# Optimization experiments

Measured on AMD Instinct MI355X. Metric: run time of the kernel, lower is better.

The kernel has to match this reference:

```python
import jax, jax.numpy as jnp
import numpy as np
from jax.ops import segment_sum

EPS = 1e-5
N, E = 100000, 1600000
CIN, H, COUT, ED = 32, 64, 16, 16


def _lin(k, fan_in, fan_out):
    return jax.random.normal(k, (fan_in, fan_out), jnp.float32) / np.sqrt(fan_in)


def setup_inputs() -> dict:
    key = jax.random.key(0)
    ks = jax.random.split(key, 24)
    inp = {
        "x": jax.random.normal(ks[0], (N, CIN), jnp.float32),
        "edge_index": jax.random.randint(ks[1], (2, E), 0, N, jnp.int32),
        "edge_attr": jax.random.normal(ks[2], (E, ED), jnp.float32),
    }
    # layer 1 (SAGEConvWithEdgeAttr: in=CIN -> H)
    inp.update(
        l1_Wl=_lin(ks[3], CIN, H), l1_bl=jnp.zeros((H,), jnp.float32),
        l1_Wr=_lin(ks[4], CIN, H),
        l1_We=_lin(ks[5], ED, H), l1_be=jnp.zeros((H,), jnp.float32),
        l1_Wg=_lin(ks[6], 2 * H, H), l1_bg=jnp.zeros((H,), jnp.float32),
        l1_bng=jnp.ones((H,), jnp.float32), l1_bnb=jnp.zeros((H,), jnp.float32),
    )
    # layer 2 (H -> H)
    inp.update(
        l2_Wl=_lin(ks[7], H, H), l2_bl=jnp.zeros((H,), jnp.float32),
        l2_Wr=_lin(ks[8], H, H),
        l2_We=_lin(ks[9], ED, H), l2_be=jnp.zeros((H,), jnp.float32),
        l2_Wg=_lin(ks[10], 2 * H, H), l2_bg=jnp.zeros((H,), jnp.float32),
        l2_bng=jnp.ones((H,), jnp.float32), l2_bnb=jnp.zeros((H,), jnp.float32),
    )
    # GraphNorms (weight=1, bias=0, mean_scale=1 at init; randomize slightly via ones)
    inp.update(
        gn1_g=jnp.ones((H,), jnp.float32), gn1_b=jnp.zeros((H,), jnp.float32), gn1_a=jnp.ones((H,), jnp.float32),
        gn2_g=jnp.ones((H,), jnp.float32), gn2_b=jnp.zeros((H,), jnp.float32), gn2_a=jnp.ones((H,), jnp.float32),
        lin_W=_lin(ks[11], H, COUT), lin_b=jnp.zeros((COUT,), jnp.float32),
    )
    return inp


def _sage_edge_layer(x, row, col, ea, Wl, bl, Wr, We, be, Wg, bg, bng, bnb):
    n = x.shape[0]
    ea_t = ea @ We + be                                        # [E', H]
    deg = segment_sum(jnp.ones_like(col, dtype=x.dtype), col, num_segments=n)
    agg = segment_sum(x[row], col, num_segments=n) / jnp.maximum(deg, 1.0)[:, None]
    out = agg @ Wl + bl + x @ Wr                               # SAGEConv (mean)
    gate = jax.nn.sigmoid(jnp.concatenate([out[col], ea_t], -1) @ Wg + bg)
    out = out + segment_sum(gate * ea_t, col, num_segments=n)  # edge contributions
    mu = out.mean(0)
    var = ((out - mu) ** 2).mean(0)                            # BatchNorm1d (batch stats)
    out = bng * (out - mu) * jax.lax.rsqrt(var + EPS) + bnb
    return jax.nn.relu(2.0 * out)                              # Identity residual + out, relu


def _graph_norm(x, g, b, a):
    mu = x.mean(0)
    xc = x - a * mu
    var = (xc ** 2).mean(0)
    return g * xc * jax.lax.rsqrt(var + EPS) + b


def reference(x, edge_index, edge_attr,
              l1_Wl, l1_bl, l1_Wr, l1_We, l1_be, l1_Wg, l1_bg, l1_bng, l1_bnb,
              l2_Wl, l2_bl, l2_Wr, l2_We, l2_be, l2_Wg, l2_bg, l2_bng, l2_bnb,
              gn1_g, gn1_b, gn1_a, gn2_g, gn2_b, gn2_a, lin_W, lin_b):
    n = x.shape[0]
    loop = jnp.arange(n, dtype=edge_index.dtype)
    row = jnp.concatenate([edge_index[0], loop])               # add_self_loops
    col = jnp.concatenate([edge_index[1], loop])
    ea = jnp.concatenate([edge_attr, jnp.ones((n, edge_attr.shape[1]), edge_attr.dtype)], 0)
    h = _sage_edge_layer(x, row, col, ea, l1_Wl, l1_bl, l1_Wr, l1_We, l1_be, l1_Wg, l1_bg, l1_bng, l1_bnb)
    h = jax.nn.relu(h)
    h = jax.nn.relu(_graph_norm(h, gn1_g, gn1_b, gn1_a))
    h = _sage_edge_layer(h, row, col, ea, l2_Wl, l2_bl, l2_Wr, l2_We, l2_be, l2_Wg, l2_bg, l2_bng, l2_bnb)
    h = jax.nn.relu(h)
    h = jax.nn.relu(_graph_norm(h, gn2_g, gn2_b, gn2_a))
    return h @ lin_W + lin_b
```

## Files before the change

kernel.cpp:

```cpp
#include <hip/hip_runtime.h>
#include <hip/hip_fp16.h>
#include <math.h>
#include <stdint.h>

#define H 64
#define ED 16
#define CO 16
#define WGRID 2048
#define NWAVES (WGRID * 4)
#define CPART 1024
static constexpr float EPSV = 1e-5f;
static constexpr float LOG2E = 1.44269504f;

typedef _Float16 h2v __attribute__((ext_vector_type(2)));
typedef _Float16 f16x8 __attribute__((ext_vector_type(8)));
typedef float f32x4 __attribute__((ext_vector_type(4)));

__device__ __forceinline__ float sigm2(float z) {
    return __builtin_amdgcn_rcpf(1.0f + __builtin_amdgcn_exp2f(-z));
}

__device__ __forceinline__ f16x8 as_f16x8(int4 v) { union { int4 i; f16x8 h; } u; u.i = v; return u.h; }

__device__ __forceinline__ int pack2(float a, float b) {
    __half2 h = __floats2half2_rn(a, b);
    return *reinterpret_cast<int*>(&h);
}

__global__ void k_prep(const float* __restrict__ We1, const float* __restrict__ be1, const float* __restrict__ Wg1,
                       const float* __restrict__ We2, const float* __restrict__ be2, const float* __restrict__ Wg2,
                       float* __restrict__ ws) {
    int j = threadIdx.x;
    for (int l = 0; l < 2; ++l) {
        const float* We = l ? We2 : We1;
        const float* be = l ? be2 : be1;
        const float* Wg = l ? Wg2 : Wg1;
        int* wth = (int*)(ws + (l ? 1024 : 0));
        int* wgh = (int*)(ws + (l ? 1536 : 512));
        float* ets = ws + 2048 + l * 192;
        float* vs  = ws + 2112 + l * 192;
        float* dv  = ws + 2176 + l * 192;
        float wt[ED], wg[ED];
        float et = be[j];
        for (int k = 0; k < ED; ++k) { wt[k] = We[k * H + j]; et += wt[k]; }
        ets[j] = et;
        float d = 0.f;
        for (int m = 0; m < H; ++m) d += be[m] * Wg[(H + m) * H + j];
        float vsum = d;
        for (int k = 0; k < ED; ++k) {
            float acc = 0.f;
            for (int m = 0; m < H; ++m) acc += We[k * H + m] * Wg[(H + m) * H + j];
            wg[k] = acc;
            vsum += acc;
        }
        dv[j] = d * LOG2E;
        vs[j] = vsum * LOG2E;
        for (int q = 0; q < 8; ++q) {
            wth[j * 8 + q] = pack2(wt[2 * q], wt[2 * q + 1]);
            wgh[j * 8 + q] = pack2(wg[2 * q] * LOG2E, wg[2 * q + 1] * LOG2E);
        }
    }
    for (int s = 0; s < 8; ++s) ws[2432 + s * 64 + j] = 0.f;
}

__global__ void k_xh(const float* __restrict__ x, __half* __restrict__ xh, int total4) {
    int i = blockIdx.x * blockDim.x + threadIdx.x;
    if (i >= total4) return;
    float4 v = *reinterpret_cast<const float4*>(x + (size_t)i * 4);
    __half2 h0 = __floats2half2_rn(v.x, v.y), h1 = __floats2half2_rn(v.z, v.w);
    uint2 o;
    o.x = *reinterpret_cast<unsigned*>(&h0);
    o.y = *reinterpret_cast<unsigned*>(&h1);
    *reinterpret_cast<uint2*>(xh + (size_t)i * 4) = o;
}

__global__ __launch_bounds__(1024) void k_scan1(const int* __restrict__ cnt, int* __restrict__ bs, int N) {
    __shared__ int ls[1024];
    int t = threadIdx.x;
    int i = blockIdx.x * 1024 + t;
    ls[t] = (i < N) ? cnt[i] : 0;
    __syncthreads();
    for (int off = 512; off > 0; off >>= 1) {
        if (t < off) ls[t] += ls[t + off];
        __syncthreads();
    }
    if (t == 0) bs[blockIdx.x] = ls[0];
}

__global__ __launch_bounds__(1024) void k_scan2(int* __restrict__ bs, int SB) {
    __shared__ int ls[1024];
    int t = threadIdx.x;
    int v = (t < SB) ? bs[t] : 0;
    ls[t] = v;
    __syncthreads();
    for (int off = 1; off < 1024; off <<= 1) {
        int x = (t >= off) ? ls[t - off] : 0;
        __syncthreads();
        ls[t] += x;
        __syncthreads();
    }
    if (t < SB) bs[t] = ls[t] - v;
}

__global__ __launch_bounds__(1024) void k_scan3(const int* __restrict__ cnt, const int* __restrict__ bs,
                                                int* __restrict__ rowptr, int N, int E) {
    __shared__ int ls[1024];
    int t = threadIdx.x;
    int i = blockIdx.x * 1024 + t;
    int v = (i < N) ? cnt[i] : 0;
    ls[t] = v;
    __syncthreads();
    for (int off = 1; off < 1024; off <<= 1) {
        int x = (t >= off) ? ls[t - off] : 0;
        __syncthreads();
        ls[t] += x;
        __syncthreads();
    }
    if (i < N) rowptr[i] = bs[blockIdx.x] + ls[t] - v;
    if (i == 0) rowptr[N] = E;
}

__global__ void k_ranges(const int* __restrict__ rowptr, int* __restrict__ ranges, int N, int E, int nw) {
    int w = blockIdx.x * blockDim.x + threadIdx.x;
    if (w > nw) return;
    if (w == nw) { ranges[nw] = N; return; }
    int t0 = (int)((long)E * w / nw);
    int lo = 0, hi = N;
    while (lo < hi) { int mid = (lo + hi) >> 1; if (rowptr[mid] < t0) lo = mid + 1; else hi = mid; }
    ranges[w] = lo;
}

__global__ __launch_bounds__(256) void k_part(const int* __restrict__ rows, const int* __restrict__ cols,
                                              const float* __restrict__ ea,
                                              int2* __restrict__ tmpk, int4* __restrict__ tmpp,
                                              int* __restrict__ offtab, int* __restrict__ cnt,
                                              int E, int NB, int SH) {
    __shared__ int hist[1025];
    __shared__ int pscan[256];
    __shared__ int2 skey[CPART];
    __shared__ int4 spay[CPART][2];
    int tid = threadIdx.x;
    int base = blockIdx.x * CPART;
    int cntE = min(CPART, E - base);
    for (int i = tid; i <= NB; i += 256) hist[i] = 0;
    __syncthreads();
    int myc[4], myr[4];
    int4 pa0[4], pa1[4];
#pragma unroll
    for (int q = 0; q < 4; ++q) {
        int li = q * 256 + tid;
        if (li < cntE) {
            int e = base + li;
            myc[q] = cols[e];
            myr[q] = rows[e];
            const float4* src = reinterpret_cast<const float4*>(ea + (size_t)e * ED);
            float4 v0 = src[0], v1 = src[1], v2 = src[2], v3 = src[3];
            int hh[8];
            hh[0] = pack2(v0.x, v0.y); hh[1] = pack2(v0.z, v0.w);
            hh[2] = pack2(v1.x, v1.y); hh[3] = pack2(v1.z, v1.w);
            hh[4] = pack2(v2.x, v2.y); hh[5] = pack2(v2.z, v2.w);
            hh[6] = pack2(v3.x, v3.y); hh[7] = pack2(v3.z, v3.w);
            pa0[q] = reinterpret_cast<const int4*>(hh)[0];
            pa1[q] = reinterpret_cast<const int4*>(hh)[1];
            atomicAdd(&hist[myc[q] >> SH], 1);
            atomicAdd(&cnt[myc[q]], 1);
        } else myc[q] = -1;
    }
    __syncthreads();
    int h[4], s = 0;
    int b0 = tid * 4;
#pragma unroll
    for (int k = 0; k < 4; ++k) { h[k] = (b0 + k < NB) ? hist[b0 + k] : 0; s += h[k]; }
    pscan[tid] = s;
    __syncthreads();
    for (int off = 1; off < 256; off <<= 1) {
        int v = (tid >= off) ? pscan[tid - off] : 0;
        __syncthreads();
        pscan[tid] += v;
        __syncthreads();
    }
    int excl = pscan[tid] - s;
    __syncthreads();
    int run = excl;
#pragma unroll
    for (int k = 0; k < 4; ++k) {
        if (b0 + k < NB) hist[b0 + k] = run;
        run += h[k];
    }
    __syncthreads();
    int* ot = offtab + (size_t)blockIdx.x * (NB + 1);
    for (int i = tid; i < NB; i += 256) ot[i] = hist[i];
    if (tid == 0) ot[NB] = cntE;
    __syncthreads();
    int mask = (1 << SH) - 1;
#pragma unroll
    for (int q = 0; q < 4; ++q) {
        if (myc[q] >= 0) {
            int b = myc[q] >> SH;
            int p = atomicAdd(&hist[b], 1);
            skey[p] = make_int2(myr[q], myc[q] & mask);
            spay[p][0] = pa0[q];
            spay[p][1] = pa1[q];
        }
    }
    __syncthreads();
    for (int i = tid; i < cntE; i += 256) {
        tmpk[base + i] = skey[i];
        tmpp[(size_t)(base + i) * 2 + 0] = spay[i][0];
        tmpp[(size_t)(base + i) * 2 + 1] = spay[i][1];
    }
}

__global__ __launch_bounds__(1024) void k_build(const int* __restrict__ rowptr, const int2* __restrict__ tmpk,
                                               const int4* __restrict__ tmpp,
                                               const int* __restrict__ offtab,
                                               int* __restrict__ erow, __half* __restrict__ eap,
                                               int N, int NB, int SH, int PB) {
    __shared__ int lcur[1024];
    int tid = threadIdx.x;
    int b = blockIdx.x;
    int NPB = 1 << SH;
    int nodelo = b << SH;
    for (int j = tid; j < NPB; j += 1024) {
        int n = nodelo + j;
        lcur[j] = (n < N) ? rowptr[n] : 0;
    }
    __syncthreads();
    for (int i = tid; i < PB; i += 1024) {
        const int* ot = offtab + (size_t)i * (NB + 1);
        int j0 = ot[b], j1 = ot[b + 1];
        for (int j = j0; j < j1; ++j) {
            size_t src = (size_t)i * CPART + j;
            int2 k = tmpk[src];
            int4 a0 = tmpp[src * 2 + 0];
            int4 a1 = tmpp[src * 2 + 1];
            int p = atomicAdd(&lcur[k.y], 1);
            erow[p] = k.x;
            int4* d = reinterpret_cast<int4*>(eap + (size_t)p * ED);
            d[0] = a0; d[1] = a1;
        }
    }
}

template <int CIN, bool GN>
__global__ __launch_bounds__(256) void k_gather(const __half* __restrict__ x, const int* __restrict__ rowptr,
                         const int* __restrict__ ranges,
                         const int* __restrict__ erow, float* __restrict__ agg,
                         const float* __restrict__ s1, const float* __restrict__ s2,
                         const float* __restrict__ gng, const float* __restrict__ gnb,
                         const float* __restrict__ gna, float Ninv, int N) {
    int lane = threadIdx.x & 63;
    int w = (blockIdx.x * blockDim.x + threadIdx.x) >> 6;
    float A = 1.f, B = 0.f;
    if (GN) {
        float mu = s1[lane] * Ninv, m2 = s2[lane] * Ninv, a = gna[lane];
        float var = m2 - 2.f * a * mu * mu + a * a * mu * mu;
        A = gng[lane] * rsqrtf(var + EPSV);
        B = gnb[lane] - A * a * mu;
    }
    int n0 = ranges[w], n1 = ranges[w + 1];
    for (int n = n0; n < n1; ++n) {
        int s = rowptr[n], te = rowptr[n + 1];
        if (CIN == 64) {
            float raw = __half2float(x[(size_t)n * 64 + lane]);
            float acc = GN ? fmaxf(fmaf(A, raw, B), 0.f) : raw;
            int i = s;
            for (; i + 7 < te; i += 8) {
                int r0 = erow[i],     r1 = erow[i + 1], r2 = erow[i + 2], r3 = erow[i + 3];
                int r4 = erow[i + 4], r5 = erow[i + 5], r6 = erow[i + 6], r7 = erow[i + 7];
                float x0 = __half2float(x[(size_t)r0 * 64 + lane]);
                float x1 = __half2float(x[(size_t)r1 * 64 + lane]);
                float x2 = __half2float(x[(size_t)r2 * 64 + lane]);
                float x3 = __half2float(x[(size_t)r3 * 64 + lane]);
                float x4 = __half2float(x[(size_t)r4 * 64 + lane]);
                float x5 = __half2float(x[(size_t)r5 * 64 + lane]);
                float x6 = __half2float(x[(size_t)r6 * 64 + lane]);
                float x7 = __half2float(x[(size_t)r7 * 64 + lane]);
                if (GN) {
                    x0 = fmaxf(fmaf(A, x0, B), 0.f); x1 = fmaxf(fmaf(A, x1, B), 0.f);
                    x2 = fmaxf(fmaf(A, x2, B), 0.f); x3 = fmaxf(fmaf(A, x3, B), 0.f);
                    x4 = fmaxf(fmaf(A, x4, B), 0.f); x5 = fmaxf(fmaf(A, x5, B), 0.f);
                    x6 = fmaxf(fmaf(A, x6, B), 0.f); x7 = fmaxf(fmaf(A, x7, B), 0.f);
                }
                acc += ((x0 + x1) + (x2 + x3)) + ((x4 + x5) + (x6 + x7));
            }
            for (; i < te; ++i) {
                float xv = __half2float(x[(size_t)erow[i] * 64 + lane]);
                if (GN) xv = fmaxf(fmaf(A, xv, B), 0.f);
                acc += xv;
            }
            agg[(size_t)n * H + lane] = acc;
        } else {
            int c = lane & 31, half = lane >> 5;
            float acc = half ? 0.f : __half2float(x[(size_t)n * 32 + c]);
            int i = s + half;
            for (; i + 6 < te; i += 8) {
                int r0 = erow[i], r1 = erow[i + 2], r2 = erow[i + 4], r3 = erow[i + 6];
                float x0 = __half2float(x[(size_t)r0 * 32 + c]);
                float x1 = __half2float(x[(size_t)r1 * 32 + c]);
                float x2 = __half2float(x[(size_t)r2 * 32 + c]);
                float x3 = __half2float(x[(size_t)r3 * 32 + c]);
                acc += (x0 + x1) + (x2 + x3);
            }
            for (; i < te; i += 2) acc += __half2float(x[(size_t)erow[i] * 32 + c]);
            acc += __shfl_xor(acc, 32);
            if (half == 0) agg[(size_t)n * H + c] = acc;
        }
    }
}

#define MT4A(mq, aval) \
    acc[mq][0] = fmaf(aval, w1.x, acc[mq][0]); acc[mq][1] = fmaf(aval, w1.y, acc[mq][1]); \
    acc[mq][2] = fmaf(aval, w1.z, acc[mq][2]); acc[mq][3] = fmaf(aval, w1.w, acc[mq][3]);
#define MT4X(mq, aval) \
    acc[mq][0] = fmaf(aval, w2.x, acc[mq][0]); acc[mq][1] = fmaf(aval, w2.y, acc[mq][1]); \
    acc[mq][2] = fmaf(aval, w2.z, acc[mq][2]); acc[mq][3] = fmaf(aval, w2.w, acc[mq][3]);

template <int K, bool GN>
__global__ __launch_bounds__(256) void k_gemmfu(
        const float* __restrict__ A,
        const __half* __restrict__ A2, int lda2,
        const float* __restrict__ W1, const float* __restrict__ W2,
        const float* __restrict__ bias,
        const float* __restrict__ Wg, const float* __restrict__ bg,
        const float* __restrict__ s1, const float* __restrict__ s2,
        const float* __restrict__ gng, const float* __restrict__ gnb,
        const float* __restrict__ gna, float Ninv,
        const int* __restrict__ rowptr,
        __half* __restrict__ pre, __half* __restrict__ uout, int N) {
    __shared__ float WA[64 * 64];
    __shared__ float WB[K * 64];
    __shared__ float big[64][68];
    __shared__ float As[64], Bs[64], invd[64];
    int tid = threadIdx.x;
    for (int idx = tid; idx < K * 64; idx += 256) { WA[idx] = W1[idx]; WB[idx] = W2[idx]; }
    int nb = blockIdx.x * 64;
    if (tid < 64) {
        if (GN) {
            float mu = s1[tid] * Ninv, m2 = s2[tid] * Ninv, a = gna[tid];
            float var = m2 - 2.f * a * mu * mu + a * a * mu * mu;
            float Av = gng[tid] * rsqrtf(var + EPSV);
            As[tid] = Av; Bs[tid] = gnb[tid] - Av * a * mu;
        }
        int n = nb + tid;
        invd[tid] = (n < N) ? 1.f / (float)(rowptr[n + 1] - rowptr[n] + 1) : 0.f;
    }
    __syncthreads();
    int tm = tid >> 4, tn = tid & 15;
    int m0 = tm * 4, j0 = tn * 4;
    float acc[4][4];
#pragma unroll
    for (int jq = 0; jq < 4; ++jq) {
        float b = bias[j0 + jq];
#pragma unroll
        for (int mq = 0; mq < 4; ++mq) acc[mq][jq] = b;
    }
    int sn = tid >> 2, kq4 = (tid & 3) * 4;
    int sg = nb + sn;
    for (int k0 = 0; k0 < K; k0 += 16) {
        if (k0) __syncthreads();
        if (sg < N) {
            float4 av = *reinterpret_cast<const float4*>(A + (size_t)sg * 64 + k0 + kq4);
            float sc = invd[sn];
            av.x *= sc; av.y *= sc; av.z *= sc; av.w *= sc;
            big[kq4 + 0][sn] = av.x; big[kq4 + 1][sn] = av.y;
            big[kq4 + 2][sn] = av.z; big[kq4 + 3][sn] = av.w;
            uint2 hv = *reinterpret_cast<const uint2*>(A2 + (size_t)sg * lda2 + k0 + kq4);
            __half2 h01 = *reinterpret_cast<__half2*>(&hv.x);
            __half2 h23 = *reinterpret_cast<__half2*>(&hv.y);
            float2 f01 = __half22float2(h01), f23 = __half22float2(h23);
            float xv0 = f01.x, xv1 = f01.y, xv2 = f23.x, xv3 = f23.y;
            if (GN) {
                xv0 = fmaxf(fmaf(As[k0 + kq4 + 0], xv0, Bs[k0 + kq4 + 0]), 0.f);
                xv1 = fmaxf(fmaf(As[k0 + kq4 + 1], xv1, Bs[k0 + kq4 + 1]), 0.f);
                xv2 = fmaxf(fmaf(As[k0 + kq4 + 2], xv2, Bs[k0 + kq4 + 2]), 0.f);
                xv3 = fmaxf(fmaf(As[k0 + kq4 + 3], xv3, Bs[k0 + kq4 + 3]), 0.f);
            }
            big[16 + kq4 + 0][sn] = xv0; big[16 + kq4 + 1][sn] = xv1;
            big[16 + kq4 + 2][sn] = xv2; big[16 + kq4 + 3][sn] = xv3;
        } else {
#pragma unroll
            for (int q = 0; q < 4; ++q) { big[kq4 + q][sn] = 0.f; big[16 + kq4 + q][sn] = 0.f; }
        }
        __syncthreads();
#pragma unroll
        for (int k = 0; k < 16; ++k) {
            float4 am = *reinterpret_cast<const float4*>(&big[k][m0]);
            float4 w1 = *reinterpret_cast<const float4*>(&WA[(k0 + k) * 64 + j0]);
            MT4A(0, am.x) MT4A(1, am.y) MT4A(2, am.z) MT4A(3, am.w)
            float4 xm = *reinterpret_cast<const float4*>(&big[16 + k][m0]);
            float4 w2 = *reinterpret_cast<const float4*>(&WB[(k0 + k) * 64 + j0]);
            MT4X(0, xm.x) MT4X(1, xm.y) MT4X(2, xm.z) MT4X(3, xm.w)
        }
    }
    __syncthreads();
#pragma unroll
    for (int mq = 0; mq < 4; ++mq) {
        int n = nb + m0 + mq;
        if (n < N) {
            uint2 o;
            o.x = pack2(acc[mq][0], acc[mq][1]);
            o.y = pack2(acc[mq][2], acc[mq][3]);
            *reinterpret_cast<uint2*>(pre + (size_t)n * 64 + j0) = o;
        }
#pragma unroll
        for (int jq = 0; jq < 4; ++jq) big[j0 + jq][m0 + mq] = acc[mq][jq];
    }
    for (int idx = tid; idx < 4096; idx += 256) WA[idx] = Wg[idx] * LOG2E;
    __syncthreads();
    float acc2[4][4];
#pragma unroll
    for (int jq = 0; jq < 4; ++jq) {
        float b = bg[j0 + jq] * LOG2E;
#pragma unroll
        for (int mq = 0; mq < 4; ++mq) acc2[mq][jq] = b;
    }
#pragma unroll 8
    for (int k = 0; k < 64; ++k) {
        float4 pm = *reinterpret_cast<const float4*>(&big[k][m0]);
        float4 w1 = *reinterpret_cast<const float4*>(&WA[k * 64 + j0]);
        acc2[0][0] = fmaf(pm.x, w1.x, acc2[0][0]); acc2[0][1] = fmaf(pm.x, w1.y, acc2[0][1]);
        acc2[0][2] = fmaf(pm.x, w1.z, acc2[0][2]); acc2[0][3] = fmaf(pm.x, w1.w, acc2[0][3]);
        acc2[1][0] = fmaf(pm.y, w1.x, acc2[1][0]); acc2[1][1] = fmaf(pm.y, w1.y, acc2[1][1]);
        acc2[1][2] = fmaf(pm.y, w1.z, acc2[1][2]); acc2[1][3] = fmaf(pm.y, w1.w, acc2[1][3]);
        acc2[2][0] = fmaf(pm.z, w1.x, acc2[2][0]); acc2[2][1] = fmaf(pm.z, w1.y, acc2[2][1]);
        acc2[2][2] = fmaf(pm.z, w1.z, acc2[2][2]); acc2[2][3] = fmaf(pm.z, w1.w, acc2[2][3]);
        acc2[3][0] = fmaf(pm.w, w1.x, acc2[3][0]); acc2[3][1] = fmaf(pm.w, w1.y, acc2[3][1]);
        acc2[3][2] = fmaf(pm.w, w1.z, acc2[3][2]); acc2[3][3] = fmaf(pm.w, w1.w, acc2[3][3]);
    }
#pragma unroll
    for (int mq = 0; mq < 4; ++mq) {
        int n = nb + m0 + mq;
        if (n < N) {
            uint2 o;
            o.x = pack2(acc2[mq][0], acc2[mq][1]);
            o.y = pack2(acc2[mq][2], acc2[mq][3]);
            *reinterpret_cast<uint2*>(uout + (size_t)n * 64 + j0) = o;
        }
    }
}

__global__ __launch_bounds__(256) void k_gate(
        const int* __restrict__ rowptr, const int* __restrict__ ranges,
        const __half* __restrict__ eap,
        const int* __restrict__ wth, const int* __restrict__ wgh,
        const float* __restrict__ be, const float* __restrict__ dv,
        const float* __restrict__ ets, const float* __restrict__ vs,
        const __half* __restrict__ u, __half* __restrict__ pre,
        float* __restrict__ s1, float* __restrict__ s2, int N) {
    __shared__ unsigned pvet[4][16][68];
    __shared__ float ls[2][4][H];
    int lane = threadIdx.x & 63;
    int wv = threadIdx.x >> 6;
    int w = (blockIdx.x << 2) | wv;
    int g = lane >> 4, li = lane & 15;
    f16x8 Bet[4], Bv[4];
#pragma unroll
    for (int c = 0; c < 4; ++c) {
        int j = c * 16 + li;
        int4 bt = make_int4(0, 0, 0, 0), bv = make_int4(0, 0, 0, 0);
        if (g < 2) {
            bt = *reinterpret_cast<const int4*>(&wth[j * 8 + g * 4]);
            bv = *reinterpret_cast<const int4*>(&wgh[j * 8 + g * 4]);
        }
        Bet[c] = as_f16x8(bt);
        Bv[c] = as_f16x8(bv);
        if (g == 2) {
            Bet[c][0] = (_Float16)be[j];
            Bv[c][0]  = (_Float16)dv[j];
        }
    }
    float ets_l = ets[lane], vs_l = vs[lane];
    int n0 = ranges[w], n1 = ranges[w + 1];
    float s = 0.f, ss = 0.f;
    if (n0 < n1) {
        const int4* gsrc = reinterpret_cast<const int4*>(eap);
        int e0 = rowptr[n0], e1 = rowptr[n1];
        int n = n0;
        int nend = rowptr[n0 + 1];
        size_t idx = (size_t)n * H + lane;
        float u_l = __half2float(u[idx]);
        float pv = __half2float(pre[idx]);
        int np = min(n + 1, n1 - 1);
        size_t idxn = (size_t)np * H + lane;
        float u_n = __half2float(u[idxn]);
        float pv_n = __half2float(pre[idxn]);
        float acc = sigm2(u_l + vs_l) * ets_l;
        int4 afr = make_int4(0, 0, 0, 0);
        {
            int ei = e0 + li;
            if (g < 2 && ei < e1) afr = gsrc[(size_t)ei * 2 + g];
        }
        for (int tb = e0; tb < e1; tb += 16) {
            int4 afc = afr;
            afr = make_int4(0, 0, 0, 0);
            {
                int ei = tb + 16 + li;
                if (g < 2 && ei < e1) afr = gsrc[(size_t)ei * 2 + g];
            }
            f16x8 Af = as_f16x8(afc);
            if (g == 2) Af[0] = (_Float16)1.0f;
            f32x4 z = {0.f, 0.f, 0.f, 0.f};
            f32x4 et0 = __builtin_amdgcn_mfma_f32_16x16x32_f16(Af, Bet[0], z, 0, 0, 0);
            f32x4 et1 = __builtin_amdgcn_mfma_f32_16x16x32_f16(Af, Bet[1], z, 0, 0, 0);
            f32x4 et2 = __builtin_amdgcn_mfma_f32_16x16x32_f16(Af, Bet[2], z, 0, 0, 0);
            f32x4 et3 = __builtin_amdgcn_mfma_f32_16x16x32_f16(Af, Bet[3], z, 0, 0, 0);
            f32x4 vv0 = __builtin_amdgcn_mfma_f32_16x16x32_f16(Af, Bv[0], z, 0, 0, 0);
            f32x4 vv1 = __builtin_amdgcn_mfma_f32_16x16x32_f16(Af, Bv[1], z, 0, 0, 0);
            f32x4 vv2 = __builtin_amdgcn_mfma_f32_16x16x32_f16(Af, Bv[2], z, 0, 0, 0);
            f32x4 vv3 = __builtin_amdgcn_mfma_f32_16x16x32_f16(Af, Bv[3], z, 0, 0, 0);
            int r0 = g * 4;
#pragma unroll
            for (int r = 0; r < 4; ++r) {
                pvet[wv][r0 + r][li]      = (unsigned)pack2(vv0[r], et0[r]);
                pvet[wv][r0 + r][16 + li] = (unsigned)pack2(vv1[r], et1[r]);
                pvet[wv][r0 + r][32 + li] = (unsigned)pack2(vv2[r], et2[r]);
                pvet[wv][r0 + r][48 + li] = (unsigned)pack2(vv3[r], et3[r]);
            }
            int pend = min(e1, tb + 16);
            int p = tb;
            while (p < pend) {
                while (p == nend) {
                    float tval = pv + acc;
                    pre[idx] = __float2half(tval);
                    s += tval; ss += tval * tval;
                    ++n;
                    idx = idxn; u_l = u_n; pv = pv_n;
                    np = min(n + 1, n1 - 1);
                    idxn = (size_t)np * H + lane;
                    u_n = __half2float(u[idxn]);
                    pv_n = __half2float(pre[idxn]);
                    acc = sigm2(u_l + vs_l) * ets_l;
                    nend = rowptr[n + 1];
                }
                int lim = min(pend, nend);
                for (; p + 1 < lim; p += 2) {
                    unsigned w0 = pvet[wv][p - tb][lane];
                    unsigned w1 = pvet[wv][p + 1 - tb][lane];
                    float2 f0 = __half22float2(*reinterpret_cast<__half2*>(&w0));
                    float2 f1 = __half22float2(*reinterpret_cast<__half2*>(&w1));
                    acc += sigm2(u_l + f0.x) * f0.y + sigm2(u_l + f1.x) * f1.y;
                }
                if (p < lim) {
                    unsigned w0 = pvet[wv][p - tb][lane];
                    float2 f0 = __half22float2(*reinterpret_cast<__half2*>(&w0));
                    acc += sigm2(u_l + f0.x) * f0.y;
                    ++p;
                }
            }
        }
        for (;;) {
            float tval = pv + acc;
            pre[idx] = __float2half(tval);
            s += tval; ss += tval * tval;
            ++n;
            if (n >= n1) break;
            idx = idxn; u_l = u_n; pv = pv_n;
            np = min(n + 1, n1 - 1);
            idxn = (size_t)np * H + lane;
            u_n = __half2float(u[idxn]);
            pv_n = __half2float(pre[idxn]);
            acc = sigm2(u_l + vs_l) * ets_l;
        }
    }
    ls[0][wv][lane] = s; ls[1][wv][lane] = ss;
    __syncthreads();
    if (threadIdx.x < H) {
        float a = ls[0][0][lane] + ls[0][1][lane] + ls[0][2][lane] + ls[0][3][lane];
        float b = ls[1][0][lane] + ls[1][1][lane] + ls[1][2][lane] + ls[1][3][lane];
        atomicAdd(&s1[lane], a);
        atomicAdd(&s2[lane], b);
    }
}

__global__ void k_apply(const __half* __restrict__ in, __half* __restrict__ outb,
                        const float* __restrict__ bng, const float* __restrict__ bnb,
                        const float* __restrict__ s1b, const float* __restrict__ s2b,
                        float* __restrict__ s1g, float* __restrict__ s2g, float Ninv, int N) {
    int j = threadIdx.x, ty = threadIdx.y;
    __shared__ float As[H], Bs[H];
    if (ty == 0) {
        float mu = s1b[j] * Ninv, var = s2b[j] * Ninv - mu * mu;
        float r = rsqrtf(var + EPSV);
        float A = 2.f * bng[j] * r;
        As[j] = A; Bs[j] = 2.f * (bnb[j] - bng[j] * r * mu);
    }
    __syncthreads();
    float A = As[j], B = Bs[j];
    float s = 0.f, ss = 0.f;
    for (int n = blockIdx.x * 4 + ty; n < N; n += gridDim.x * 4) {
        size_t idx = (size_t)n * H + j;
        float v = fmaxf(fmaf(A, __half2float(in[idx]), B), 0.f);
        outb[idx] = __float2half(v);
        s += v; ss += v * v;
    }
    __shared__ float ls[2][4][H];
    ls[0][ty][j] = s; ls[1][ty][j] = ss;
    __syncthreads();
    if (ty == 0) {
        float a = ls[0][0][j] + ls[0][1][j] + ls[0][2][j] + ls[0][3][j];
        float b = ls[1][0][j] + ls[1][1][j] + ls[1][2][j] + ls[1][3][j];
        atomicAdd(&s1g[j], a);
        atomicAdd(&s2g[j], b);
    }
}

__global__ __launch_bounds__(256) void k_final(const __half* __restrict__ hraw, const float* __restrict__ W,
                        const float* __restrict__ bias,
                        const float* __restrict__ s1, const float* __restrict__ s2,
                        const float* __restrict__ gng, const float* __restrict__ gnb,
                        const float* __restrict__ gna, float Ninv,
                        float* __restrict__ outp, int N) {
    __shared__ float As[H], Bs[H];
    if (threadIdx.x < H) {
        int j = threadIdx.x;
        float mu = s1[j] * Ninv, m2 = s2[j] * Ninv, a = gna[j];
        float var = m2 - 2.f * a * mu * mu + a * a * mu * mu;
        float A = gng[j] * rsqrtf(var + EPSV);
        As[j] = A; Bs[j] = gnb[j] - A * a * mu;
    }
    __syncthreads();
    int n = blockIdx.x * blockDim.x + threadIdx.x;
    if (n >= N) return;
    float o[CO];
#pragma unroll
    for (int t = 0; t < CO; ++t) o[t] = bias[t];
    const __half* hr = hraw + (size_t)n * H;
    for (int m4 = 0; m4 < H / 4; ++m4) {
        uint2 hv = *reinterpret_cast<const uint2*>(hr + m4 * 4);
        __half2 h01 = *reinterpret_cast<__half2*>(&hv.x);
        __half2 h23 = *reinterpret_cast<__half2*>(&hv.y);
        float2 f01 = __half22float2(h01), f23 = __half22float2(h23);
        float hx = fmaxf(fmaf(As[m4*4+0], f01.x, Bs[m4*4+0]), 0.f);
        float hy = fmaxf(fmaf(As[m4*4+1], f01.y, Bs[m4*4+1]), 0.f);
        float hz = fmaxf(fmaf(As[m4*4+2], f23.x, Bs[m4*4+2]), 0.f);
        float hw = fmaxf(fmaf(As[m4*4+3], f23.y, Bs[m4*4+3]), 0.f);
#pragma unroll
        for (int t = 0; t < CO; ++t) {
            o[t] += hx * W[(m4*4+0) * CO + t];
            o[t] += hy * W[(m4*4+1) * CO + t];
            o[t] += hz * W[(m4*4+2) * CO + t];
            o[t] += hw * W[(m4*4+3) * CO + t];
        }
    }
    float* orow = outp + (size_t)n * CO;
#pragma unroll
    for (int t4 = 0; t4 < CO / 4; ++t4)
        reinterpret_cast<float4*>(orow)[t4] = make_float4(o[t4*4+0], o[t4*4+1], o[t4*4+2], o[t4*4+3]);
}

extern "C" void kernel_launch(void* const* d_in, const int* in_sizes, int n_in,
                              void* d_out, int out_size, void* d_ws, size_t ws_size,
                              hipStream_t stream) {
    const float* x     = (const float*)d_in[0];
    const int*   ei    = (const int*)d_in[1];
    const float* ea    = (const float*)d_in[2];
    const float* l1_Wl = (const float*)d_in[3];  const float* l1_bl = (const float*)d_in[4];
    const float* l1_Wr = (const float*)d_in[5];  const float* l1_We = (const float*)d_in[6];
    const float* l1_be = (const float*)d_in[7];  const float* l1_Wg = (const float*)d_in[8];
    const float* l1_bg = (const float*)d_in[9];  const float* l1_bng= (const float*)d_in[10];
    const float* l1_bnb= (const float*)d_in[11];
    const float* l2_Wl = (const float*)d_in[12]; const float* l2_bl = (const float*)d_in[13];
    const float* l2_Wr = (const float*)d_in[14]; const float* l2_We = (const float*)d_in[15];
    const float* l2_be = (const float*)d_in[16]; const float* l2_Wg = (const float*)d_in[17];
    const float* l2_bg = (const float*)d_in[18]; const float* l2_bng= (const float*)d_in[19];
    const float* l2_bnb= (const float*)d_in[20];
    const float* gn1_g = (const float*)d_in[21]; const float* gn1_b = (const float*)d_in[22];
    const float* gn1_a = (const float*)d_in[23];
    const float* gn2_g = (const float*)d_in[24]; const float* gn2_b = (const float*)d_in[25];
    const float* gn2_a = (const float*)d_in[26];
    const float* lin_W = (const float*)d_in[27]; const float* lin_b = (const float*)d_in[28];

    const int N = in_sizes[0] / 32;
    const int E = in_sizes[1] / 2;
    const int* rows = ei;
    const int* cols = ei + E;

    int SH = 7, NPB = 128;
    while (((N + NPB - 1) >> SH) > 1024) { SH++; NPB <<= 1; }
    const int NB = (N + NPB - 1) >> SH;
    const int PB = (E + CPART - 1) / CPART;

    float* w    = (float*)d_ws;
    int* wth1   = (int*)w;
    int* wgh1   = (int*)(w + 512);
    int* wth2   = (int*)(w + 1024);
    int* wgh2   = (int*)(w + 1536);
    float* ets1 = w + 2048; float* vs1 = w + 2112; float* dv1 = w + 2176;
    float* ets2 = w + 2240; float* vs2 = w + 2304; float* dv2 = w + 2368;
    float* stats= w + 2432;

    int* ip     = (int*)(w + 8192);
    int* rowptr = ip;
    int* cnt    = ip + (N + 1);
    int* bs     = cnt + N;
    int* ranges = bs + 1024;
    int* erow   = ranges + (NWAVES + 2);

    uintptr_t pa = (uintptr_t)(erow + E);
    pa = (pa + 255) & ~(uintptr_t)255;
    __half* eap = (__half*)pa;
    uintptr_t px = (uintptr_t)(eap + (size_t)E * ED);
    px = (px + 255) & ~(uintptr_t)255;
    __half* xh = (__half*)px;
    uintptr_t pz = (uintptr_t)(xh + (size_t)N * 32);
    pz = (pz + 255) & ~(uintptr_t)255;

    int2* tmpk  = (int2*)pz;
    int4* tmpp  = (int4*)(tmpk + E);
    int* offtab = (int*)(tmpp + (size_t)E * 2);

    size_t NB64 = (size_t)N * H;
    float* B0 = (float*)pz;
    __half* Bpre = (__half*)(B0 + NB64);
    __half* Bu   = Bpre + NB64;
    __half* B3h  = Bu + NB64;
    __half* B0h  = (__half*)B0;

    const float Ninv = 1.0f / (float)N;
    dim3 rb(64, 4);
    int ngrid = (N + 255) / 256;
    int g64 = (N + 63) / 64;
    const int SB = (N + 1023) >> 10;

    k_prep<<<1, 64, 0, stream>>>(l1_We, l1_be, l1_Wg, l2_We, l2_be, l2_Wg, w);
    k_xh<<<(N * 8 + 255) / 256, 256, 0, stream>>>(x, xh, N * 8);

    hipMemsetAsync(cnt, 0, sizeof(int) * (size_t)N, stream);
    k_part<<<PB, 256, 0, stream>>>(rows, cols, ea, tmpk, tmpp, offtab, cnt, E, NB, SH);
    k_scan1<<<SB, 1024, 0, stream>>>(cnt, bs, N);
    k_scan2<<<1, 1024, 0, stream>>>(bs, SB);
    k_scan3<<<SB, 1024, 0, stream>>>(cnt, bs, rowptr, N, E);
    k_ranges<<<(NWAVES + 256) / 256, 256, 0, stream>>>(rowptr, ranges, N, E, NWAVES);
    k_build<<<NB, 1024, 0, stream>>>(rowptr, tmpk, tmpp, offtab, erow, eap, N, NB, SH, PB);

    k_gather<32, false><<<WGRID, 256, 0, stream>>>(xh, rowptr, ranges, erow, B0,
                                                   nullptr, nullptr, nullptr, nullptr, nullptr, 0.f, N);
    k_gemmfu<32, false><<<g64, 256, 0, stream>>>(B0, xh, 32, l1_Wl, l1_Wr, l1_bl, l1_Wg, l1_bg,
                                                 nullptr, nullptr, nullptr, nullptr, nullptr, 0.f,
                                                 rowptr, Bpre, Bu, N);
    k_gate<<<WGRID, 256, 0, stream>>>(rowptr, ranges, eap, wth1, wgh1, l1_be, dv1, ets1, vs1,
                                      Bu, Bpre, stats + 0, stats + 64, N);
    k_apply<<<256, rb, 0, stream>>>(Bpre, B3h, l1_bng, l1_bnb, stats + 0, stats + 64,
                                    stats + 128, stats + 192, Ninv, N);

    k_gather<64, true><<<WGRID, 256, 0, stream>>>(B3h, rowptr, ranges, erow, B0,
                                                  stats + 128, stats + 192, gn1_g, gn1_b, gn1_a, Ninv, N);
    k_gemmfu<64, true><<<g64, 256, 0, stream>>>(B0, B3h, 64, l2_Wl, l2_Wr, l2_bl, l2_Wg, l2_bg,
                                                stats + 128, stats + 192, gn1_g, gn1_b, gn1_a, Ninv,
                                                rowptr, Bpre, Bu, N);
    k_gate<<<WGRID, 256, 0, stream>>>(rowptr, ranges, eap, wth2, wgh2, l2_be, dv2, ets2, vs2,
                                      Bu, Bpre, stats + 256, stats + 320, N);
    k_apply<<<256, rb, 0, stream>>>(Bpre, B0h, l2_bng, l2_bnb, stats + 256, stats + 320,
                                    stats + 384, stats + 448, Ninv, N);

    k_final<<<ngrid, 256, 0, stream>>>(B0h, lin_W, lin_b, stats + 384, stats + 448,
                                       gn2_g, gn2_b, gn2_a, Ninv, (float*)d_out, N);
}
```

Measured before the change: 644.1 us.

## Store gather aggregates in fp16, unroll gather 16-wide, vectorize k_apply

Measured after the change: 607.2 us. 5.7% less time.

```diff
diff --git a/kernel.cpp b/kernel.cpp
--- a/kernel.cpp
+++ b/kernel.cpp
@@ -245,7 +245,7 @@
 template <int CIN, bool GN>
 __global__ __launch_bounds__(256) void k_gather(const __half* __restrict__ x, const int* __restrict__ rowptr,
                          const int* __restrict__ ranges,
-                         const int* __restrict__ erow, float* __restrict__ agg,
+                         const int* __restrict__ erow, __half* __restrict__ agg,
                          const float* __restrict__ s1, const float* __restrict__ s2,
                          const float* __restrict__ gng, const float* __restrict__ gnb,
                          const float* __restrict__ gna, float Ninv, int N) {
@@ -265,31 +265,43 @@
             float raw = __half2float(x[(size_t)n * 64 + lane]);
             float acc = GN ? fmaxf(fmaf(A, raw, B), 0.f) : raw;
             int i = s;
+            for (; i + 15 < te; i += 16) {
+                float xv[16];
+#pragma unroll
+                for (int q = 0; q < 16; ++q)
+                    xv[q] = __half2float(x[(size_t)erow[i + q] * 64 + lane]);
+                float t0 = 0.f, t1 = 0.f;
+#pragma unroll
+                for (int q = 0; q < 16; q += 2) {
+                    float a0 = xv[q], a1 = xv[q + 1];
+                    if (GN) {
+                        a0 = fmaxf(fmaf(A, a0, B), 0.f);
+                        a1 = fmaxf(fmaf(A, a1, B), 0.f);
+                    }
+                    t0 += a0; t1 += a1;
+                }
+                acc += t0 + t1;
+            }
             for (; i + 7 < te; i += 8) {
-                int r0 = erow[i],     r1 = erow[i + 1], r2 = erow[i + 2], r3 = erow[i + 3];
-                int r4 = erow[i + 4], r5 = erow[i + 5], r6 = erow[i + 6], r7 = erow[i + 7];
-                float x0 = __half2float(x[(size_t)r0 * 64 + lane]);
-                float x1 = __half2float(x[(size_t)r1 * 64 + lane]);
-                float x2 = __half2float(x[(size_t)r2 * 64 + lane]);
-                float x3 = __half2float(x[(size_t)r3 * 64 + lane]);
-                float x4 = __half2float(x[(size_t)r4 * 64 + lane]);
-                float x5 = __half2float(x[(size_t)r5 * 64 + lane]);
-                float x6 = __half2float(x[(size_t)r6 * 64 + lane]);
-                float x7 = __half2float(x[(size_t)r7 * 64 + lane]);
-                if (GN) {
-                    x0 = fmaxf(fmaf(A, x0, B), 0.f); x1 = fmaxf(fmaf(A, x1, B), 0.f);
-                    x2 = fmaxf(fmaf(A, x2, B), 0.f); x3 = fmaxf(fmaf(A, x3, B), 0.f);
-                    x4 = fmaxf(fmaf(A, x4, B), 0.f); x5 = fmaxf(fmaf(A, x5, B), 0.f);
-                    x6 = fmaxf(fmaf(A, x6, B), 0.f); x7 = fmaxf(fmaf(A, x7, B), 0.f);
+                float xv[8];
+#pragma unroll
+                for (int q = 0; q < 8; ++q)
+                    xv[q] = __half2float(x[(size_t)erow[i + q] * 64 + lane]);
+                float t0 = 0.f;
+#pragma unroll
+                for (int q = 0; q < 8; ++q) {
+                    float a0 = xv[q];
+                    if (GN) a0 = fmaxf(fmaf(A, a0, B), 0.f);
+                    t0 += a0;
                 }
-                acc += ((x0 + x1) + (x2 + x3)) + ((x4 + x5) + (x6 + x7));
+                acc += t0;
             }
             for (; i < te; ++i) {
                 float xv = __half2float(x[(size_t)erow[i] * 64 + lane]);
                 if (GN) xv = fmaxf(fmaf(A, xv, B), 0.f);
                 acc += xv;
             }
-            agg[(size_t)n * H + lane] = acc;
+            agg[(size_t)n * H + lane] = __float2half(acc);
         } else {
             int c = lane & 31, half = lane >> 5;
             float acc = half ? 0.f : __half2float(x[(size_t)n * 32 + c]);
@@ -304,7 +316,7 @@
             }
             for (; i < te; i += 2) acc += __half2float(x[(size_t)erow[i] * 32 + c]);
             acc += __shfl_xor(acc, 32);
-            if (half == 0) agg[(size_t)n * H + c] = acc;
+            if (half == 0) agg[(size_t)n * H + c] = __float2half(acc);
         }
     }
 }
@@ -318,7 +330,7 @@
 
 template <int K, bool GN>
 __global__ __launch_bounds__(256) void k_gemmfu(
-        const float* __restrict__ A,
+        const __half* __restrict__ A,
         const __half* __restrict__ A2, int lda2,
         const float* __restrict__ W1, const float* __restrict__ W2,
         const float* __restrict__ bias,
@@ -360,11 +372,13 @@
     for (int k0 = 0; k0 < K; k0 += 16) {
         if (k0) __syncthreads();
         if (sg < N) {
-            float4 av = *reinterpret_cast<const float4*>(A + (size_t)sg * 64 + k0 + kq4);
+            uint2 av2 = *reinterpret_cast<const uint2*>(A + (size_t)sg * 64 + k0 + kq4);
+            __half2 a01 = *reinterpret_cast<__half2*>(&av2.x);
+            __half2 a23 = *reinterpret_cast<__half2*>(&av2.y);
+            float2 fa01 = __half22float2(a01), fa23 = __half22float2(a23);
             float sc = invd[sn];
-            av.x *= sc; av.y *= sc; av.z *= sc; av.w *= sc;
-            big[kq4 + 0][sn] = av.x; big[kq4 + 1][sn] = av.y;
-            big[kq4 + 2][sn] = av.z; big[kq4 + 3][sn] = av.w;
+            big[kq4 + 0][sn] = fa01.x * sc; big[kq4 + 1][sn] = fa01.y * sc;
+            big[kq4 + 2][sn] = fa23.x * sc; big[kq4 + 3][sn] = fa23.y * sc;
             uint2 hv = *reinterpret_cast<const uint2*>(A2 + (size_t)sg * lda2 + k0 + kq4);
             __half2 h01 = *reinterpret_cast<__half2*>(&hv.x);
             __half2 h23 = *reinterpret_cast<__half2*>(&hv.y);
@@ -573,35 +587,52 @@
     }
 }
 
-__global__ void k_apply(const __half* __restrict__ in, __half* __restrict__ outb,
+__global__ __launch_bounds__(256) void k_apply(const __half* __restrict__ in, __half* __restrict__ outb,
                         const float* __restrict__ bng, const float* __restrict__ bnb,
                         const float* __restrict__ s1b, const float* __restrict__ s2b,
                         float* __restrict__ s1g, float* __restrict__ s2g, float Ninv, int N) {
-    int j = threadIdx.x, ty = threadIdx.y;
+    int tid = threadIdx.x;
+    int cg = (tid & 15) * 4;
+    int ty = tid >> 4;
     __shared__ float As[H], Bs[H];
-    if (ty == 0) {
-        float mu = s1b[j] * Ninv, var = s2b[j] * Ninv - mu * mu;
+    __shared__ float red[2][16][H];
+    if (tid < 64) {
+        float mu = s1b[tid] * Ninv, var = s2b[tid] * Ninv - mu * mu;
         float r = rsqrtf(var + EPSV);
-        float A = 2.f * bng[j] * r;
-        As[j] = A; Bs[j] = 2.f * (bnb[j] - bng[j] * r * mu);
-    }
-    __syncthreads();
-    float A = As[j], B = Bs[j];
-    float s = 0.f, ss = 0.f;
-    for (int n = blockIdx.x * 4 + ty; n < N; n += gridDim.x * 4) {
-        size_t idx = (size_t)n * H + j;
-        float v = fmaxf(fmaf(A, __half2float(in[idx]), B), 0.f);
-        outb[idx] = __float2half(v);
-        s += v; ss += v * v;
-    }
-    __shared__ float ls[2][4][H];
-    ls[0][ty][j] = s; ls[1][ty][j] = ss;
-    __syncthreads();
-    if (ty == 0) {
-        float a = ls[0][0][j] + ls[0][1][j] + ls[0][2][j] + ls[0][3][j];
-        float b = ls[1][0][j] + ls[1][1][j] + ls[1][2][j] + ls[1][3][j];
-        atomicAdd(&s1g[j], a);
-        atomicAdd(&s2g[j], b);
+        float A = 2.f * bng[tid] * r;
+        As[tid] = A; Bs[tid] = 2.f * (bnb[tid] - bng[tid] * r * mu);
+    }
+    __syncthreads();
+    float A0 = As[cg], A1 = As[cg + 1], A2 = As[cg + 2], A3 = As[cg + 3];
+    float B0 = Bs[cg], B1 = Bs[cg + 1], B2 = Bs[cg + 2], B3 = Bs[cg + 3];
+    float s0 = 0.f, s1_ = 0.f, s2_ = 0.f, s3 = 0.f;
+    float q0 = 0.f, q1 = 0.f, q2 = 0.f, q3 = 0.f;
+    for (int n = blockIdx.x * 16 + ty; n < N; n += gridDim.x * 16) {
+        size_t idx = (size_t)n * H + cg;
+        uint2 hv = *reinterpret_cast<const uint2*>(in + idx);
+        __half2 h01 = *reinterpret_cast<__half2*>(&hv.x);
+        __half2 h23 = *reinterpret_cast<__half2*>(&hv.y);
+        float2 f01 = __half22float2(h01), f23 = __half22float2(h23);
+        float v0 = fmaxf(fmaf(A0, f01.x, B0), 0.f);
+        float v1 = fmaxf(fmaf(A1, f01.y, B1), 0.f);
+        float v2 = fmaxf(fmaf(A2, f23.x, B2), 0.f);
+        float v3 = fmaxf(fmaf(A3, f23.y, B3), 0.f);
+        uint2 o;
+        o.x = (unsigned)pack2(v0, v1);
+        o.y = (unsigned)pack2(v2, v3);
+        *reinterpret_cast<uint2*>(outb + idx) = o;
+        s0 += v0; s1_ += v1; s2_ += v2; s3 += v3;
+        q0 += v0 * v0; q1 += v1 * v1; q2 += v2 * v2; q3 += v3 * v3;
+    }
+    *reinterpret_cast<float4*>(&red[0][ty][cg]) = make_float4(s0, s1_, s2_, s3);
+    *reinterpret_cast<float4*>(&red[1][ty][cg]) = make_float4(q0, q1, q2, q3);
+    __syncthreads();
+    if (tid < H) {
+        float a = 0.f, b = 0.f;
+#pragma unroll
+        for (int r = 0; r < 16; ++r) { a += red[0][r][tid]; b += red[1][r][tid]; }
+        atomicAdd(&s1g[tid], a);
+        atomicAdd(&s2g[tid], b);
     }
 }
 
@@ -711,14 +742,13 @@
     int* offtab = (int*)(tmpp + (size_t)E * 2);
 
     size_t NB64 = (size_t)N * H;
-    float* B0 = (float*)pz;
-    __half* Bpre = (__half*)(B0 + NB64);
+    __half* Bagg = (__half*)pz;
+    __half* Bpre = Bagg + NB64;
     __half* Bu   = Bpre + NB64;
     __half* B3h  = Bu + NB64;
-    __half* B0h  = (__half*)B0;
+    __half* B0h  = Bagg;
 
     const float Ninv = 1.0f / (float)N;
-    dim3 rb(64, 4);
     int ngrid = (N + 255) / 256;
     int g64 = (N + 63) / 64;
     const int SB = (N + 1023) >> 10;
@@ -734,25 +764,25 @@
     k_ranges<<<(NWAVES + 256) / 256, 256, 0, stream>>>(rowptr, ranges, N, E, NWAVES);
     k_build<<<NB, 1024, 0, stream>>>(rowptr, tmpk, tmpp, offtab, erow, eap, N, NB, SH, PB);
 
-    k_gather<32, false><<<WGRID, 256, 0, stream>>>(xh, rowptr, ranges, erow, B0,
+    k_gather<32, false><<<WGRID, 256, 0, stream>>>(xh, rowptr, ranges, erow, Bagg,
                                                    nullptr, nullptr, nullptr, nullptr, nullptr, 0.f, N);
-    k_gemmfu<32, false><<<g64, 256, 0, stream>>>(B0, xh, 32, l1_Wl, l1_Wr, l1_bl, l1_Wg, l1_bg,
+    k_gemmfu<32, false><<<g64, 256, 0, stream>>>(Bagg, xh, 32, l1_Wl, l1_Wr, l1_bl, l1_Wg, l1_bg,
                                                  nullptr, nullptr, nullptr, nullptr, nullptr, 0.f,
                                                  rowptr, Bpre, Bu, N);
     k_gate<<<WGRID, 256, 0, stream>>>(rowptr, ranges, eap, wth1, wgh1, l1_be, dv1, ets1, vs1,
                                       Bu, Bpre, stats + 0, stats + 64, N);
-    k_apply<<<256, rb, 0, stream>>>(Bpre, B3h, l1_bng, l1_bnb, stats + 0, stats + 64,
-                                    stats + 128, stats + 192, Ninv, N);
-
-    k_gather<64, true><<<WGRID, 256, 0, stream>>>(B3h, rowptr, ranges, erow, B0,
+    k_apply<<<256, 256, 0, stream>>>(Bpre, B3h, l1_bng, l1_bnb, stats + 0, stats + 64,
+                                     stats + 128, stats + 192, Ninv, N);
+
+    k_gather<64, true><<<WGRID, 256, 0, stream>>>(B3h, rowptr, ranges, erow, Bagg,
                                                   stats + 128, stats + 192, gn1_g, gn1_b, gn1_a, Ninv, N);
-    k_gemmfu<64, true><<<g64, 256, 0, stream>>>(B0, B3h, 64, l2_Wl, l2_Wr, l2_bl, l2_Wg, l2_bg,
+    k_gemmfu<64, true><<<g64, 256, 0, stream>>>(Bagg, B3h, 64, l2_Wl, l2_Wr, l2_bl, l2_Wg, l2_bg,
                                                 stats + 128, stats + 192, gn1_g, gn1_b, gn1_a, Ninv,
                                                 rowptr, Bpre, Bu, N);
     k_gate<<<WGRID, 256, 0, stream>>>(rowptr, ranges, eap, wth2, wgh2, l2_be, dv2, ets2, vs2,
                                       Bu, Bpre, stats + 256, stats + 320, N);
-    k_apply<<<256, rb, 0, stream>>>(Bpre, B0h, l2_bng, l2_bnb, stats + 256, stats + 320,
-                                    stats + 384, stats + 448, Ninv, N);
+    k_apply<<<256, 256, 0, stream>>>(Bpre, B0h, l2_bng, l2_bnb, stats + 256, stats + 320,
+                                     stats + 384, stats + 448, Ninv, N);
 
     k_final<<<ngrid, 256, 0, stream>>>(B0h, lin_W, lin_b, stats + 384, stats + 448,
                                        gn2_g, gn2_b, gn2_a, Ninv, (float*)d_out, N);
```
